# Performance work log

Hardware: AMD Instinct MI355X
Metric: run time of the kernel (lower is better)

## Reference

```python
import jax, jax.numpy as jnp
import numpy as np

B, T, D = 2, 2048, 1024
NH, NKV, HD = 16, 4, 64
ROPE = 16  # partial RoPE dims (first 16 of 64)
HALF = ROPE // 2


def apply_rope(x, cos, sin):
    # x: (B, nH, T, HD); rotate first ROPE dims, pass the rest through
    x1 = x[..., :HALF]
    x2 = x[..., HALF:ROPE]
    xp = x[..., ROPE:]
    c = cos[None, None, :, :]  # (1,1,T,HALF)
    s = sin[None, None, :, :]
    return jnp.concatenate([x1 * c - x2 * s, x1 * s + x2 * c, xp], axis=-1)


def setup_inputs() -> dict:
    key = jax.random.key(0)
    k0, k1, k2 = jax.random.split(key, 3)
    x = jax.random.normal(k0, (B, T, D), dtype=jnp.float32)
    # RoPE tables for the rotated sub-dimension (half = ROPE//2 = 8)
    inv_freq = 1.0 / (10000.0 ** (jnp.arange(HALF, dtype=jnp.float32) / HALF))
    ang = jnp.arange(T, dtype=jnp.float32)[:, None] * inv_freq[None, :]
    cos = jnp.cos(ang)
    sin = jnp.sin(ang)
    attn_mask = jnp.tril(jnp.ones((T, T), dtype=bool))  # causal
    w_qkv = jax.random.normal(k1, ((NH + 2 * NKV) * HD, D), dtype=jnp.float32) * (D ** -0.5)
    w_out = jax.random.normal(k2, (D, D), dtype=jnp.float32) * (D ** -0.5)
    q_scale = jnp.full((NH, 1), 1.5, dtype=jnp.float32)
    k_scale = jnp.full((NKV, 1), 1.5, dtype=jnp.float32)
    return {"x": x, "cos": cos, "sin": sin, "attn_mask": attn_mask,
            "w_qkv": w_qkv, "w_out": w_out, "q_scale": q_scale, "k_scale": k_scale}


def reference(x, cos, sin, attn_mask, w_qkv, w_out, q_scale, k_scale):
    Bx, Tx, C = x.shape
    groups = NH // NKV
    qkv = x @ w_qkv.T  # (B,T,(NH+2*NKV)*HD)
    q, k, v = jnp.split(qkv, [NH * HD, (NH + NKV) * HD], axis=-1)
    q = q.reshape(Bx, Tx, NH, HD).transpose(0, 2, 1, 3)    # (B,NH,T,HD)
    k = k.reshape(Bx, Tx, NKV, HD).transpose(0, 2, 1, 3)   # (B,NKV,T,HD)
    v = v.reshape(Bx, Tx, NKV, HD).transpose(0, 2, 1, 3)
    # per-head qk gain scaling
    q = q * q_scale[None, :, :, None]  # (1,NH,1,1)
    k = k * k_scale[None, :, :, None]
    # partial RoPE on q and k
    q = apply_rope(q, cos[:Tx], sin[:Tx])
    k = apply_rope(k, cos[:Tx], sin[:Tx])
    # GQA expand (repeat_interleave along heads)
    ke = jnp.repeat(k, groups, axis=1)  # (B,NH,T,HD)
    ve = jnp.repeat(v, groups, axis=1)
    # scaled dot-product attention with causal mask
    scores = jnp.einsum('bhqd,bhkd->bhqk', q, ke) * (HD ** -0.5)
    scores = jnp.where(attn_mask[None, None], scores, -jnp.inf)
    probs = jax.nn.softmax(scores, axis=-1)
    ao = jnp.einsum('bhqk,bhkd->bhqd', probs, ve)  # (B,NH,T,HD)
    # xsa: subtract self-component along the (shared) kv value direction
    ao_r = ao.reshape(Bx, NKV, groups, Tx, HD)
    vv = v[:, :, None]  # (B,NKV,1,T,HD), broadcasts over groups
    dots = jnp.sum(ao_r * vv, axis=-1, keepdims=True)
    norm = jnp.maximum(jnp.sum(vv * vv, axis=-1, keepdims=True), 1e-8)
    ao = (ao_r - (dots / norm) * vv).reshape(Bx, NH, Tx, HD)
    out = ao.transpose(0, 2, 1, 3).reshape(Bx, Tx, C) @ w_out.T
    return out
```

## Files before the change

### kernel.cpp

```cpp
#include <hip/hip_runtime.h>
#include <hip/hip_bf16.h>

#define NB 2
#define NT 2048
#define ND 1024
#define NHEADS 16
#define NKVH 4
#define HDIM 64
#define QKVD 1536

typedef __attribute__((ext_vector_type(8))) short short8;
typedef __attribute__((ext_vector_type(4))) float floatx4;

#if defined(__has_builtin)
#  if __has_builtin(__builtin_amdgcn_global_load_lds)
#    define HAS_GLL 1
#  endif
#endif
#ifndef HAS_GLL
#  define HAS_GLL 0
#endif

__device__ __forceinline__ void gll16(const void* g, void* l, int lane) {
#if HAS_GLL
  (void)lane;
  __builtin_amdgcn_global_load_lds(
      (const __attribute__((address_space(1))) unsigned int*)g,
      (__attribute__((address_space(3))) unsigned int*)l, 16, 0, 0);
#else
  *(short8*)((short*)l) = *(const short8*)g;
#endif
}

__device__ __forceinline__ unsigned short f2bf(float f) {
  union { float f; unsigned int u; } cv; cv.f = f;
  unsigned int u = cv.u;
  u += 0x7fffu + ((u >> 16) & 1u);
  return (unsigned short)(u >> 16);
}
__device__ __forceinline__ float bf2f(unsigned short u) {
  union { unsigned int u; float f; } cv; cv.u = ((unsigned int)u) << 16; return cv.f;
}

#define N4_X   1048576
#define N4_WQ   393216
#define N4_WO   262144
__global__ __launch_bounds__(256) void cvt_all(
    const float* __restrict__ x, const float* __restrict__ wq,
    const float* __restrict__ wo,
    unsigned short* __restrict__ xb, unsigned short* __restrict__ wqb,
    unsigned short* __restrict__ wob) {
  int i = blockIdx.x * 256 + threadIdx.x;
  const float* src; unsigned short* dst; int j;
  if (i < N4_X)              { src = x;  dst = xb;  j = i; }
  else if (i < N4_X + N4_WQ) { src = wq; dst = wqb; j = i - N4_X; }
  else                       { src = wo; dst = wob; j = i - N4_X - N4_WQ; }
  float4 v = ((const float4*)src)[j];
  ushort4 o;
  o.x = f2bf(v.x); o.y = f2bf(v.y); o.z = f2bf(v.z); o.w = f2bf(v.w);
  ((ushort4*)dst)[j] = o;
}


#define GEMM1W_PROLOGUE(Aptr, Bptr, Kdim)                                      \
  __shared__ __align__(16) short As[2][64][32];                                \
  __shared__ __align__(16) short Bs[2][64][32];                                \
  const int lane = threadIdx.x;                                                \
  const int quad = lane >> 4, l16 = lane & 15;                                 \
  const int srow = lane >> 2;                                                  \
  const int sch  = ((lane & 3) ^ (srow & 3)) * 8;                              \
  const unsigned short* agp = (Aptr) + (size_t)(m0 + srow) * (Kdim) + sch;     \
  const unsigned short* bgp = (Bptr) + (size_t)(n0 + srow) * (Kdim) + sch;     \
  short* asb = &As[0][0][0];                                                   \
  short* bsb = &Bs[0][0][0];                                                   \
  const int lofs = (HAS_GLL ? 0 : lane * 8);                                   \
  const int cs = (quad ^ (l16 & 3)) * 8;                                       \
  floatx4 acc[4][4] = {};                                                      \
  _Pragma("unroll")                                                            \
  for (int g = 0; g < 4; g++) {                                                \
    gll16(agp + (size_t)(16 * g) * (Kdim), asb + g * 512 + lofs, lane);        \
    gll16(bgp + (size_t)(16 * g) * (Kdim), bsb + g * 512 + lofs, lane);        \
  }                                                                            \
  const int NIT = (Kdim) / 32;                                                 \
  for (int it = 0; it < NIT; it++) {                                           \
    __syncthreads();                                                           \
    const int bi = it & 1, bn = bi ^ 1;                                        \
    if (it + 1 < NIT) {                                                        \
      const int k = (it + 1) * 32;                                             \
      _Pragma("unroll")                                                        \
      for (int g = 0; g < 4; g++) {                                            \
        gll16(agp + (size_t)(16 * g) * (Kdim) + k, asb + bn * 2048 + g * 512 + lofs, lane); \
        gll16(bgp + (size_t)(16 * g) * (Kdim) + k, bsb + bn * 2048 + g * 512 + lofs, lane); \
      }                                                                        \
    }                                                                          \
    short8 af[4], bf[4];                                                       \
    _Pragma("unroll")                                                          \
    for (int mi = 0; mi < 4; mi++) af[mi] = *(const short8*)&As[bi][mi * 16 + l16][cs]; \
    _Pragma("unroll")                                                          \
    for (int ni = 0; ni < 4; ni++) bf[ni] = *(const short8*)&Bs[bi][ni * 16 + l16][cs]; \
    _Pragma("unroll")                                                          \
    for (int mi = 0; mi < 4; mi++)                                             \
      _Pragma("unroll")                                                        \
      for (int ni = 0; ni < 4; ni++)                                           \
        acc[mi][ni] = __builtin_amdgcn_mfma_f32_16x16x32_bf16(af[mi], bf[ni], acc[mi][ni], 0, 0, 0); \
  }

__global__ __launch_bounds__(64) void gemm_qkv(
    const unsigned short* __restrict__ A,
    const unsigned short* __restrict__ Bm,
    const float* __restrict__ cosT, const float* __restrict__ sinT,
    const float* __restrict__ q_scale, const float* __restrict__ k_scale,
    unsigned short* __restrict__ qb, unsigned short* __restrict__ kb,
    unsigned short* __restrict__ vtb)
{
  const int m0 = blockIdx.x * 64, n0 = blockIdx.y * 64;
  GEMM1W_PROLOGUE(A, Bm, ND)

  const int hh = blockIdx.y;
  const int lo8 = l16 & 7;

  if (hh >= NHEADS + NKVH) {
    const int kvh = hh - (NHEADS + NKVH);
#pragma unroll
    for (int mi = 0; mi < 4; mi++) {
      const int mrow = m0 + mi * 16 + quad * 4;
      const int bb = mrow >> 11, tt = mrow & (NT - 1);
#pragma unroll
      for (int ni = 0; ni < 4; ni++) {
        const int d = ni * 16 + l16;
        ushort4 w;
        w.x = f2bf(acc[mi][ni][0]); w.y = f2bf(acc[mi][ni][1]);
        w.z = f2bf(acc[mi][ni][2]); w.w = f2bf(acc[mi][ni][3]);
        *(ushort4*)(vtb + ((size_t)((bb * NKVH + kvh) * HDIM + d)) * NT + tt) = w;
      }
    }
  } else {
    float scl; unsigned short* dst0; int hloc, nh;
    if (hh < NHEADS) { scl = q_scale[hh] * (0.125f * 1.44269504088896f); hloc = hh; dst0 = qb; nh = NHEADS; }
    else             { scl = k_scale[hh - NHEADS]; hloc = hh - NHEADS; dst0 = kb; nh = NKVH; }
#pragma unroll
    for (int mi = 0; mi < 4; mi++) {
#pragma unroll
      for (int r = 0; r < 4; r++) {
        const int mrow = m0 + mi * 16 + quad * 4 + r;
        const int bb = mrow >> 11, tt = mrow & (NT - 1);
        unsigned short* drow = dst0 + ((size_t)((bb * nh + hloc) * NT + tt)) * HDIM;

        const float own = acc[mi][0][r];
        const float oth = __shfl_xor(own, 8);
        const float c = cosT[tt * 8 + lo8], s = sinT[tt * 8 + lo8];
        const float roped = (l16 < 8) ? (own * c - oth * s)
                                      : (oth * s + own * c);
        drow[l16] = f2bf(roped * scl);
#pragma unroll
        for (int ni = 1; ni < 4; ni++)
          drow[ni * 16 + l16] = f2bf(acc[mi][ni][r] * scl);
      }
    }
  }
}

__global__ __launch_bounds__(64) void gemm_out(
    const unsigned short* __restrict__ A,
    const unsigned short* __restrict__ Bm,
    float* __restrict__ C, int M, int N, int K)
{
  const int m0 = blockIdx.x * 64, n0 = blockIdx.y * 64;
  GEMM1W_PROLOGUE(A, Bm, K)

#pragma unroll
  for (int mi = 0; mi < 4; mi++)
#pragma unroll
    for (int ni = 0; ni < 4; ni++)
#pragma unroll
      for (int r = 0; r < 4; r++) {
        int m = m0 + mi * 16 + quad * 4 + r;
        int n = n0 + ni * 16 + l16;
        C[(size_t)m * N + n] = acc[mi][ni][r];
      }
}

__global__ __launch_bounds__(256) void fattn(
    const unsigned short* __restrict__ qb,
    const unsigned short* __restrict__ kb,
    const unsigned short* __restrict__ vtb,
    unsigned short* __restrict__ aob,
    float* __restrict__ pbuf)
{
  const int idx = blockIdx.x;
  const int h = blockIdx.y, b = blockIdx.z;
  const int kv = h >> 2;

  int qt, j0, cnt, chunk; bool direct;
  if (idx < 16) { qt = 16 + idx; j0 = 0; cnt = 16; chunk = 0; direct = false; }
  else {
    int rel = idx - 16, s = 16 - (rel >> 1);
    if ((rel & 1) == 0) { qt = s - 1;  j0 = 0;  cnt = s; chunk = 0; direct = true;  }
    else                { qt = s + 15; j0 = 16; cnt = s; chunk = 1; direct = false; }
  }

  const int tid = threadIdx.x;
  const int wid = tid >> 6, lane = tid & 63;
  const int quad = lane >> 4, l16 = lane & 15;
  const int hi8 = l16 >> 3, lo8 = l16 & 7;

  __shared__ __align__(16) short Ks[2][64][64];
  __shared__ __align__(16) short Vs[2][64][64];
  __shared__ __align__(16) short Ps[4][16][64];

  const unsigned short* qg = qb + ((size_t)((b * NHEADS + h) * NT + qt * 64)) * HDIM;
  const int qrow = wid * 16 + l16;
  short8 aq0 = *(const short8*)(qg + (size_t)qrow * HDIM + quad * 8);
  short8 aq1 = *(const short8*)(qg + (size_t)qrow * HDIM + 32 + quad * 8);

  const int sr  = tid >> 3;
  const int lck = ((tid & 7) ^ (sr & 7)) * 8;
  const unsigned short* kgp0 = kb  + ((size_t)((b * NKVH + kv) * NT) + sr) * HDIM + lck;
  const unsigned short* vgp0 = vtb + ((size_t)((b * NKVH + kv) * HDIM) + sr) * NT + lck;
  short* ksb = &Ks[0][0][0];
  short* vsb = &Vs[0][0][0];
  const int lofs = (HAS_GLL ? wid * 512 : tid * 8);

  const int cs0 = (quad ^ lo8) * 8;
  const int cs1 = cs0 ^ 32;

  int pwo[4][4];
#pragma unroll
  for (int r = 0; r < 4; r++) {
    const int row = quad * 4 + r;
#pragma unroll
    for (int nb = 0; nb < 4; nb++)
      pwo[r][nb] = wid * 1024 + row * 64 + (((nb * 2 + hi8) ^ (row & 7)) * 8) + lo8;
  }
  short* psf = &Ps[0][0][0];

  floatx4 acc_o[4] = {};
  float lsum[4] = {0.f, 0.f, 0.f, 0.f};

  {
    const unsigned short* kg = kgp0 + (size_t)j0 * 64 * HDIM;
    const unsigned short* vg = vgp0 + j0 * 64;
    gll16(kg, ksb + lofs, lane);
    gll16(kg + 32 * HDIM, ksb + 2048 + lofs, lane);
    gll16(vg, vsb + lofs, lane);
    gll16(vg + (size_t)32 * NT, vsb + 2048 + lofs, lane);
  }

  for (int i = 0; i < cnt; i++) {
    const int jt = j0 + i;
    __syncthreads();
    const int bi = i & 1, bn = bi ^ 1;
    if (i + 1 < cnt) {
      const unsigned short* kg = kgp0 + (size_t)(jt + 1) * 64 * HDIM;
      const unsigned short* vg = vgp0 + (jt + 1) * 64;
      gll16(kg, ksb + bn * 4096 + lofs, lane);
      gll16(kg + 32 * HDIM, ksb + bn * 4096 + 2048 + lofs, lane);
      gll16(vg, vsb + bn * 4096 + lofs, lane);
      gll16(vg + (size_t)32 * NT, vsb + bn * 4096 + 2048 + lofs, lane);
    }

    floatx4 s[4] = {};
#pragma unroll
    for (int nb = 0; nb < 4; nb++) {
      short8 bk0 = *(const short8*)&Ks[bi][nb * 16 + l16][cs0];
      short8 bk1 = *(const short8*)&Ks[bi][nb * 16 + l16][cs1];
      s[nb] = __builtin_amdgcn_mfma_f32_16x16x32_bf16(aq0, bk0, s[nb], 0, 0, 0);
      s[nb] = __builtin_amdgcn_mfma_f32_16x16x32_bf16(aq1, bk1, s[nb], 0, 0, 0);
    }

    if (jt == qt) {
#pragma unroll
      for (int nb = 0; nb < 4; nb++) {
        int col = nb * 16 + l16;
#pragma unroll
        for (int r = 0; r < 4; r++)
          if (col > wid * 16 + quad * 4 + r) s[nb][r] = -INFINITY;
      }
    }

#pragma unroll
    for (int r = 0; r < 4; r++) {
#pragma unroll
      for (int nb = 0; nb < 4; nb++) {
        float p = __builtin_amdgcn_exp2f(s[nb][r]);
        lsum[r] += p;
        psf[pwo[r][nb]] = (short)(__float_as_uint(p) >> 16);
      }
    }

    short8 ap0 = *(const short8*)&Ps[wid][l16][cs0];
    short8 ap1 = *(const short8*)&Ps[wid][l16][cs1];
#pragma unroll
    for (int nb = 0; nb < 4; nb++) {
      short8 bv0 = *(const short8*)&Vs[bi][nb * 16 + l16][cs0];
      short8 bv1 = *(const short8*)&Vs[bi][nb * 16 + l16][cs1];
      acc_o[nb] = __builtin_amdgcn_mfma_f32_16x16x32_bf16(ap0, bv0, acc_o[nb], 0, 0, 0);
      acc_o[nb] = __builtin_amdgcn_mfma_f32_16x16x32_bf16(ap1, bv1, acc_o[nb], 0, 0, 0);
    }
  }

  const int bl = (cnt - 1) & 1;

  if (direct) {
#pragma unroll
    for (int r = 0; r < 4; r++) {
      float ls = lsum[r];
#pragma unroll
      for (int off = 1; off < 16; off <<= 1) ls += __shfl_xor(ls, off);
      const float invl = 1.f / ls;

      const int rowl = wid * 16 + quad * 4 + r;
      const int vcol = ((rowl >> 3) ^ lo8) * 8 + (rowl & 7);
      float vd[4], dot = 0.f, vv = 0.f;
#pragma unroll
      for (int nb = 0; nb < 4; nb++) {
        vd[nb] = bf2f((unsigned short)Vs[bl][nb * 16 + l16][vcol]);
        dot += acc_o[nb][r] * invl * vd[nb];
        vv  += vd[nb] * vd[nb];
      }
#pragma unroll
      for (int off = 1; off < 16; off <<= 1) {
        dot += __shfl_xor(dot, off);
        vv  += __shfl_xor(vv, off);
      }
      const float coef = dot / fmaxf(vv, 1e-8f);
      unsigned short* dst = aob + ((size_t)(b * NT + qt * 64 + rowl)) * ND + h * HDIM + l16;
#pragma unroll
      for (int nb = 0; nb < 4; nb++)
        dst[nb * 16] = f2bf(acc_o[nb][r] * invl - coef * vd[nb]);
    }
  } else {
    const int slot = ((b * NHEADS + h) * 16 + (qt - 16)) * 2 + chunk;
    float* pO = pbuf + (size_t)slot * 4160;
    float* pl = pO + 4096;
#pragma unroll
    for (int r = 0; r < 4; r++) {
      float ls = lsum[r];
#pragma unroll
      for (int off = 1; off < 16; off <<= 1) ls += __shfl_xor(ls, off);
      const int rowl = wid * 16 + quad * 4 + r;
      if (l16 == 0) pl[rowl] = ls;
#pragma unroll
      for (int nb = 0; nb < 4; nb++)
        pO[rowl * 64 + nb * 16 + l16] = acc_o[nb][r];
    }
  }
}

__global__ __launch_bounds__(256) void redn(
    const float* __restrict__ pbuf,
    const unsigned short* __restrict__ vtb,
    unsigned short* __restrict__ aob)
{
  const int qt = 16 + blockIdx.x;
  const int h = blockIdx.y, b = blockIdx.z;
  const int kv = h >> 2;
  const int tid = threadIdx.x;

  const int slot0 = ((b * NHEADS + h) * 16 + blockIdx.x) * 2;
  const float* O0 = pbuf + (size_t)slot0 * 4160;
  const float* O1 = O0 + 4160;
  const float* l0 = O0 + 4096;
  const float* l1 = O1 + 4096;

  __shared__ short vt[64][66];

  {
    const int d = tid >> 2, tq = (tid & 3) * 16;
    const unsigned short* src = vtb + ((size_t)((b * NKVH + kv) * HDIM + d)) * NT + qt * 64 + tq;
    short8 v0 = *(const short8*)src;
    short8 v1 = *(const short8*)(src + 8);
    *(short8*)&vt[d][tq] = v0;
    *(short8*)&vt[d][tq + 8] = v1;
  }
  __syncthreads();

  const int row = tid >> 2, dq = tid & 3;
  const float invl = 1.f / (l0[row] + l1[row]);

  float o[16], vd[16];
  float dot = 0.f, vv = 0.f;
#pragma unroll
  for (int j = 0; j < 16; j++) {
    const int d = dq * 16 + j;
    float ov = (O0[row * 64 + d] + O1[row * 64 + d]) * invl;
    float v  = bf2f((unsigned short)vt[d][row]);
    o[j] = ov; vd[j] = v;
    dot += ov * v; vv += v * v;
  }
  dot += __shfl_xor(dot, 1); dot += __shfl_xor(dot, 2);
  vv  += __shfl_xor(vv, 1);  vv  += __shfl_xor(vv, 2);
  const float coef = dot / fmaxf(vv, 1e-8f);

  unsigned short* dst = aob + ((size_t)(b * NT + qt * 64 + row)) * ND + h * HDIM + dq * 16;
  ushort4 w0, w1, w2, w3;
  w0.x = f2bf(o[0] - coef * vd[0]);  w0.y = f2bf(o[1] - coef * vd[1]);
  w0.z = f2bf(o[2] - coef * vd[2]);  w0.w = f2bf(o[3] - coef * vd[3]);
  w1.x = f2bf(o[4] - coef * vd[4]);  w1.y = f2bf(o[5] - coef * vd[5]);
  w1.z = f2bf(o[6] - coef * vd[6]);  w1.w = f2bf(o[7] - coef * vd[7]);
  w2.x = f2bf(o[8] - coef * vd[8]);  w2.y = f2bf(o[9] - coef * vd[9]);
  w2.z = f2bf(o[10] - coef * vd[10]); w2.w = f2bf(o[11] - coef * vd[11]);
  w3.x = f2bf(o[12] - coef * vd[12]); w3.y = f2bf(o[13] - coef * vd[13]);
  w3.z = f2bf(o[14] - coef * vd[14]); w3.w = f2bf(o[15] - coef * vd[15]);
  ((ushort4*)dst)[0] = w0; ((ushort4*)dst)[1] = w1;
  ((ushort4*)dst)[2] = w2; ((ushort4*)dst)[3] = w3;
}

extern "C" void kernel_launch(void* const* d_in, const int* in_sizes, int n_in,
                              void* d_out, int out_size, void* d_ws, size_t ws_size,
                              hipStream_t stream) {
  const float* x       = (const float*)d_in[0];
  const float* cosT    = (const float*)d_in[1];
  const float* sinT    = (const float*)d_in[2];
  const float* w_qkv   = (const float*)d_in[4];
  const float* w_out   = (const float*)d_in[5];
  const float* q_scale = (const float*)d_in[6];
  const float* k_scale = (const float*)d_in[7];
  float* out = (float*)d_out;

  char* ws = (char*)d_ws;
  unsigned short* xb    = (unsigned short*)ws;
  unsigned short* wqkvb = (unsigned short*)(ws + 8388608);
  float*          pbuf  = (float*)ws;
  unsigned short* woutb = (unsigned short*)(ws + 17825792);
  unsigned short* qb    = (unsigned short*)(ws + 19922944);
  unsigned short* kb    = (unsigned short*)(ws + 28311552);
  unsigned short* vtb   = (unsigned short*)(ws + 30408704);
  unsigned short* aob   = (unsigned short*)(ws + 32505856);

  cvt_all<<<(N4_X + N4_WQ + N4_WO) / 256, 256, 0, stream>>>(
      x, w_qkv, w_out, xb, wqkvb, woutb);

  gemm_qkv<<<dim3(NB * NT / 64, QKVD / 64), 64, 0, stream>>>(
      xb, wqkvb, cosT, sinT, q_scale, k_scale, qb, kb, vtb);

  fattn<<<dim3(48, NHEADS, NB), 256, 0, stream>>>(qb, kb, vtb, aob, pbuf);
  redn<<<dim3(16, NHEADS, NB), 256, 0, stream>>>(pbuf, vtb, aob);

  gemm_out<<<dim3(NB * NT / 64, ND / 64), 64, 0, stream>>>(
      aob, woutb, out, NB * NT, ND, ND);
}
```

Baseline: 192.8 us.

## Transpose QK^T MFMA so lanes own query rows, pack P to bf16 vector stores

Swaps the MFMA operands for the score product so each lane holds four consecutive keys for a single query row. The row sum then accumulates in one scalar per lane and needs only two cross-quad shuffles. P values are converted to bf16 in pairs with v_cvt_pk_bf16_f32 (round-to-nearest instead of truncation) and written as 8-byte vector stores under a new swizzled LDS layout, replacing 16 scalar short stores per tile. The causal mask indexing and the final normalisation are rewritten to match the transposed fragment layout, using a shuffle to fetch each row's sum.

```diff
diff --git a/kernel.cpp b/kernel.cpp
--- a/kernel.cpp
+++ b/kernel.cpp
@@ -202,7 +202,7 @@
   const int tid = threadIdx.x;
   const int wid = tid >> 6, lane = tid & 63;
   const int quad = lane >> 4, l16 = lane & 15;
-  const int hi8 = l16 >> 3, lo8 = l16 & 7;
+  const int lo8 = l16 & 7;
 
   __shared__ __align__(16) short Ks[2][64][64];
   __shared__ __align__(16) short Vs[2][64][64];
@@ -224,18 +224,16 @@
   const int cs0 = (quad ^ lo8) * 8;
   const int cs1 = cs0 ^ 32;
 
-  int pwo[4][4];
-#pragma unroll
-  for (int r = 0; r < 4; r++) {
-    const int row = quad * 4 + r;
-#pragma unroll
-    for (int nb = 0; nb < 4; nb++)
-      pwo[r][nb] = wid * 1024 + row * 64 + (((nb * 2 + hi8) ^ (row & 7)) * 8) + lo8;
-  }
-  short* psf = &Ps[0][0][0];
+  char* psb = (char*)&Ps[0][0][0];
+  int psw[4];
+#pragma unroll
+  for (int nb = 0; nb < 4; nb++)
+    psw[nb] = wid * 2048 + l16 * 128 +
+              ((((nb << 1) | (quad >> 1)) ^ lo8) << 4) + ((quad & 1) << 3);
+  const int pr0 = wid * 2048 + l16 * 128 + ((quad ^ lo8) << 4);
 
   floatx4 acc_o[4] = {};
-  float lsum[4] = {0.f, 0.f, 0.f, 0.f};
+  float lsum = 0.f;
 
   {
     const unsigned short* kg = kgp0 + (size_t)j0 * 64 * HDIM;
@@ -264,32 +262,35 @@
     for (int nb = 0; nb < 4; nb++) {
       short8 bk0 = *(const short8*)&Ks[bi][nb * 16 + l16][cs0];
       short8 bk1 = *(const short8*)&Ks[bi][nb * 16 + l16][cs1];
-      s[nb] = __builtin_amdgcn_mfma_f32_16x16x32_bf16(aq0, bk0, s[nb], 0, 0, 0);
-      s[nb] = __builtin_amdgcn_mfma_f32_16x16x32_bf16(aq1, bk1, s[nb], 0, 0, 0);
+      s[nb] = __builtin_amdgcn_mfma_f32_16x16x32_bf16(bk0, aq0, s[nb], 0, 0, 0);
+      s[nb] = __builtin_amdgcn_mfma_f32_16x16x32_bf16(bk1, aq1, s[nb], 0, 0, 0);
     }
 
     if (jt == qt) {
-#pragma unroll
-      for (int nb = 0; nb < 4; nb++) {
-        int col = nb * 16 + l16;
+      const int qloc = wid * 16 + l16;
+#pragma unroll
+      for (int nb = 0; nb < 4; nb++)
 #pragma unroll
         for (int r = 0; r < 4; r++)
-          if (col > wid * 16 + quad * 4 + r) s[nb][r] = -INFINITY;
-      }
-    }
-
-#pragma unroll
-    for (int r = 0; r < 4; r++) {
-#pragma unroll
-      for (int nb = 0; nb < 4; nb++) {
-        float p = __builtin_amdgcn_exp2f(s[nb][r]);
-        lsum[r] += p;
-        psf[pwo[r][nb]] = (short)(__float_as_uint(p) >> 16);
-      }
-    }
-
-    short8 ap0 = *(const short8*)&Ps[wid][l16][cs0];
-    short8 ap1 = *(const short8*)&Ps[wid][l16][cs1];
+          if (nb * 16 + quad * 4 + r > qloc) s[nb][r] = -INFINITY;
+    }
+
+#pragma unroll
+    for (int nb = 0; nb < 4; nb++) {
+      float p0 = __builtin_amdgcn_exp2f(s[nb][0]);
+      float p1 = __builtin_amdgcn_exp2f(s[nb][1]);
+      float p2 = __builtin_amdgcn_exp2f(s[nb][2]);
+      float p3 = __builtin_amdgcn_exp2f(s[nb][3]);
+      lsum += (p0 + p1) + (p2 + p3);
+      unsigned int pk0, pk1;
+      asm("v_cvt_pk_bf16_f32 %0, %1, %2" : "=v"(pk0) : "v"(p0), "v"(p1));
+      asm("v_cvt_pk_bf16_f32 %0, %1, %2" : "=v"(pk1) : "v"(p2), "v"(p3));
+      uint2 w; w.x = pk0; w.y = pk1;
+      *(uint2*)(psb + psw[nb]) = w;
+    }
+
+    short8 ap0 = *(const short8*)(psb + pr0);
+    short8 ap1 = *(const short8*)(psb + (pr0 ^ 64));
 #pragma unroll
     for (int nb = 0; nb < 4; nb++) {
       short8 bv0 = *(const short8*)&Vs[bi][nb * 16 + l16][cs0];
@@ -301,15 +302,16 @@
 
   const int bl = (cnt - 1) & 1;
 
+  float lst = lsum;
+  lst += __shfl_xor(lst, 16);
+  lst += __shfl_xor(lst, 32);
+
   if (direct) {
 #pragma unroll
     for (int r = 0; r < 4; r++) {
-      float ls = lsum[r];
-#pragma unroll
-      for (int off = 1; off < 16; off <<= 1) ls += __shfl_xor(ls, off);
-      const float invl = 1.f / ls;
-
       const int rowl = wid * 16 + quad * 4 + r;
+      const float invl = 1.f / __shfl(lst, quad * 4 + r);
+
       const int vcol = ((rowl >> 3) ^ lo8) * 8 + (rowl & 7);
       float vd[4], dot = 0.f, vv = 0.f;
 #pragma unroll
@@ -333,13 +335,10 @@
     const int slot = ((b * NHEADS + h) * 16 + (qt - 16)) * 2 + chunk;
     float* pO = pbuf + (size_t)slot * 4160;
     float* pl = pO + 4096;
+    if (quad == 0) pl[wid * 16 + l16] = lst;
 #pragma unroll
     for (int r = 0; r < 4; r++) {
-      float ls = lsum[r];
-#pragma unroll
-      for (int off = 1; off < 16; off <<= 1) ls += __shfl_xor(ls, off);
       const int rowl = wid * 16 + quad * 4 + r;
-      if (l16 == 0) pl[rowl] = ls;
 #pragma unroll
       for (int nb = 0; nb < 4; nb++)
         pO[rowl * 64 + nb * 16 + l16] = acc_o[nb][r];
```

After: 190.7 us. Within noise of the previous version (-1.1%).
